# Kernel optimization log

Hardware: AMD Instinct MI355X
Metric: run time of the kernel (lower is better)

Reference implementation:

```python
import jax, jax.numpy as jnp
import numpy as np

B = 128
NHEAD = 16
D_MODEL = 512
D_IN = 256  # each of f_* and f_*_out; concat -> 512
N_ATOM = 128


def _scopes():
    lens = np.array([96 + (i % 33) for i in range(B)], dtype=np.int64)  # max == 128 == N_ATOM
    starts_a = np.concatenate([[1], 1 + np.cumsum(lens)[:-1]]).astype(np.int64)
    nb = 2 * lens
    starts_b = np.concatenate([[1], 1 + np.cumsum(nb)[:-1]]).astype(np.int64)
    return lens, starts_a, nb, starts_b


def setup_inputs() -> dict:
    key = jax.random.key(0)
    ks = jax.random.split(key, 10)
    lens, starts_a, nb, starts_b = _scopes()
    Na = int(1 + lens.sum())   # 14279 (row 0 is padding)
    Nb = int(1 + nb.sum())     # 28557 (bond 0 is padding)
    f_atoms = jax.random.normal(ks[0], (Na, D_IN), jnp.float32)
    f_bonds = jax.random.normal(ks[1], (Nb, D_IN), jnp.float32)
    f_atoms_out = jax.random.normal(ks[2], (Na, D_IN), jnp.float32)
    f_bonds_out = jax.random.normal(ks[3], (Nb, D_IN), jnp.float32)
    b2a = jax.random.randint(ks[4], (Nb,), 0, 96, jnp.int64 if jax.config.jax_enable_x64 else jnp.int32)
    b2revb = jax.random.randint(ks[5], (Nb,), 0, Nb, b2a.dtype)
    a_scope = jnp.stack([jnp.asarray(starts_a), jnp.asarray(lens)], axis=1)
    b_scope = jnp.stack([jnp.asarray(starts_b), jnp.asarray(nb)], axis=1)
    W_atom = jax.random.normal(ks[6], (2 * D_IN, D_MODEL), jnp.float32) * 0.02
    b_atom = jnp.zeros((D_MODEL,), jnp.float32)
    W_bond = jax.random.normal(ks[7], (2 * D_IN, NHEAD), jnp.float32) * 0.02
    b_bond = jnp.zeros((NHEAD,), jnp.float32)
    return {"f_atoms": f_atoms, "f_bonds": f_bonds, "f_atoms_out": f_atoms_out,
            "f_bonds_out": f_bonds_out, "b2a": b2a, "b2revb": b2revb,
            "a_scope": a_scope, "b_scope": b_scope, "n_atom": N_ATOM,
            "W_atom": W_atom, "b_atom": b_atom, "W_bond": W_bond, "b_bond": b_bond}


def reference(f_atoms, f_bonds, f_atoms_out, f_bonds_out, b2a, b2revb,
              a_scope, b_scope, n_atom, W_atom, b_atom, W_bond, b_bond):
    Bsz = a_scope.shape[0]
    # atom embedding: concat + linear, drop padding row 0, pad per-molecule -> [n_atom, B, d]
    atoms = jnp.concatenate([f_atoms, f_atoms_out], axis=1) @ W_atom + b_atom  # [Na, d]
    starts_a, lens_a = a_scope[:, 0], a_scope[:, 1]
    pos = jnp.arange(n_atom)
    valid = pos[None, :] < lens_a[:, None]                       # [B, n_atom]
    gidx = jnp.where(valid, starts_a[:, None] + pos[None, :], 0)  # safe gather idx
    atoms_pad = jnp.where(valid[..., None], atoms[gidx], 0.0)     # [B, n_atom, d]
    atoms_emb = atoms_pad.transpose(1, 0, 2)                      # [n_atom, B, d] (batch_first=False)
    # bond embedding -> scatter into dense pairwise matrix
    bonds = jnp.concatenate([f_bonds, f_bonds_out], axis=1) @ W_bond + b_bond  # [Nb, nhead]
    Nb = bonds.shape[0]
    starts_b = b_scope[:, 0]
    mol = jnp.searchsorted(starts_b, jnp.arange(Nb), side='right') - 1  # molecule id per bond (-1 for pad bond 0)
    offset = jnp.maximum(mol, 0) * (n_atom * n_atom)
    idx = b2a + b2a[b2revb] * n_atom + offset                     # flat index into [B*n_atom*n_atom]
    flat = jnp.zeros((Bsz * n_atom * n_atom, bonds.shape[1]), bonds.dtype).at[idx].set(bonds)
    apairs = flat.reshape(Bsz, n_atom, n_atom, -1)                # [B, n_atom, n_atom, nhead]
    padding_mask = ~valid                                         # [B, n_atom], True = pad
    apairs = jnp.where(padding_mask[:, None, :, None], -jnp.inf, apairs)
    apairs = apairs.transpose(0, 3, 1, 2)                         # [B, nhead, n_atom, n_atom]
    return atoms_emb, apairs, padding_mask
```

## Files before the change

### kernel.cpp

```cpp
#include <hip/hip_runtime.h>
#include <math.h>

#define NEG_BIG (-1e30f)

typedef __attribute__((ext_vector_type(8))) short short8;
typedef __attribute__((ext_vector_type(8))) _Float16 half8;
typedef __attribute__((ext_vector_type(4))) float floatx4;

__device__ __forceinline__ unsigned short f2bf(float x) {
    unsigned u = __float_as_uint(x);
    unsigned r = (u + 0x7fffu + ((u >> 16) & 1u)) >> 16;
    return (unsigned short)r;
}
__device__ __forceinline__ short f2h(float x) {
    _Float16 h = (_Float16)x;
    return __builtin_bit_cast(short, h);
}
__device__ __forceinline__ float h2f(short s) {
    return (float)__builtin_bit_cast(_Float16, s);
}

__global__ __launch_bounds__(256) void k_prep(
    const float* __restrict__ W, short* __restrict__ H, short* __restrict__ L,
    const float* __restrict__ Wb, short* __restrict__ Wbt,
    int* __restrict__ winner,
    const int* __restrict__ a_scope, float* __restrict__ mask_out, int Bmol)
{
    int bid = blockIdx.x;
    int tid = threadIdx.x;
    if (bid < 1024) {
        int t = bid * 256 + tid;
        int n = t >> 9, k = t & 511;
        float x = W[(size_t)k * 512 + n];
        short h = f2h(x);
        float r = (x - h2f(h)) * 2048.0f;
        H[t] = h;
        L[t] = f2h(r);
        return;
    }
    bid -= 1024;
    if (bid < 32) {
        int t = bid * 256 + tid;
        int h = t >> 9, k = t & 511;
        Wbt[t] = (short)f2bf(Wb[(size_t)k * 16 + h]);
        return;
    }
    bid -= 32;
    if (bid < Bmol * 16) {
        int t = bid * 256 + tid;
        ((int4*)winner)[t] = make_int4(-1, -1, -1, -1);
        return;
    }
    bid -= Bmol * 16;
    {
        int t = bid * 256 + tid;
        if (t < Bmol * 128) {
            int b = t >> 7, p = t & 127;
            mask_out[t] = (p >= a_scope[2 * b + 1]) ? 1.0f : 0.0f;
        }
    }
}


__device__ __forceinline__ void atoms_body(
    int abid, char* smem,
    const float* __restrict__ fA, const float* __restrict__ fAo,
    const int* __restrict__ a_scope,
    const short* __restrict__ WH, const short* __restrict__ WL,
    const float* __restrict__ bias, float* __restrict__ out, int Bmol)
{
    short* A_s = (short*)smem;
    short* B_s = (short*)(smem + 20480);
    int*   rs  = (int*)(smem + 40960);

    const int tid = threadIdx.x;
    const int n0 = (abid & 3) * 128;
    const int mol = abid >> 2;

    if (tid < 128) {
        int len = a_scope[2 * mol + 1];
        rs[tid] = (tid < len) ? (a_scope[2 * mol] + tid) : -1;
    }
    const int wid = tid >> 6, lane = tid & 63;
    const int wm = (wid >> 1) * 64, wn = (wid & 1) * 64;
    const int quad = lane >> 4, l16 = lane & 15;

    floatx4 acc1[4][4], acc2[4][4];
#pragma unroll
    for (int i = 0; i < 4; i++)
#pragma unroll
        for (int j = 0; j < 4; j++) {
            acc1[i][j] = (floatx4){0.f, 0.f, 0.f, 0.f};
            acc2[i][j] = (floatx4){0.f, 0.f, 0.f, 0.f};
        }

    const int ar = tid >> 1;
    const int ak = (tid & 1) * 16;
    __syncthreads();
    const int asrc = rs[ar];

    for (int k0 = 0; k0 < 512; k0 += 32) {
        float x[16];
        if (asrc >= 0) {
            int kg = k0 + ak;
            const float* p = (kg < 256) ? (fA + (size_t)asrc * 256 + kg)
                                        : (fAo + (size_t)asrc * 256 + (kg - 256));
#pragma unroll
            for (int i = 0; i < 4; i++) {
                float4 v = ((const float4*)p)[i];
                x[i * 4 + 0] = v.x; x[i * 4 + 1] = v.y;
                x[i * 4 + 2] = v.z; x[i * 4 + 3] = v.w;
            }
        } else {
#pragma unroll
            for (int i = 0; i < 16; i++) x[i] = 0.f;
        }
        size_t goff = (size_t)(n0 + ar) * 512 + k0 + ak;
        short8 bh0 = *(const short8*)(WH + goff);
        short8 bh1 = *(const short8*)(WH + goff + 8);
        short8 bl0 = *(const short8*)(WL + goff);
        short8 bl1 = *(const short8*)(WL + goff + 8);

        short8 ah0, ah1, al0, al1;
#pragma unroll
        for (int i = 0; i < 8; i++) {
            short h = f2h(x[i]);
            float r = (x[i] - h2f(h)) * 2048.0f;
            ah0[i] = h; al0[i] = f2h(r);
        }
#pragma unroll
        for (int i = 0; i < 8; i++) {
            float xx = x[8 + i];
            short h = f2h(xx);
            float r = (xx - h2f(h)) * 2048.0f;
            ah1[i] = h; al1[i] = f2h(r);
        }

        __syncthreads();
        const int abase = ar * 40 + ak;
        *(short8*)&A_s[abase] = ah0;          *(short8*)&A_s[abase + 8] = ah1;
        *(short8*)&A_s[5120 + abase] = al0;   *(short8*)&A_s[5120 + abase + 8] = al1;
        *(short8*)&B_s[abase] = bh0;          *(short8*)&B_s[abase + 8] = bh1;
        *(short8*)&B_s[5120 + abase] = bl0;   *(short8*)&B_s[5120 + abase + 8] = bl1;
        __syncthreads();

        half8 afh[4], afl[4];
#pragma unroll
        for (int ti = 0; ti < 4; ti++) {
            int off = (wm + ti * 16 + l16) * 40 + quad * 8;
            afh[ti] = *(const half8*)&A_s[off];
            afl[ti] = *(const half8*)&A_s[5120 + off];
        }
#pragma unroll
        for (int tj = 0; tj < 4; tj++) {
            int off = (wn + tj * 16 + l16) * 40 + quad * 8;
            half8 bh = *(const half8*)&B_s[off];
            half8 bl = *(const half8*)&B_s[5120 + off];
#pragma unroll
            for (int ti = 0; ti < 4; ti++) {
                acc1[ti][tj] = __builtin_amdgcn_mfma_f32_16x16x32_f16(afh[ti], bh, acc1[ti][tj], 0, 0, 0);
                acc2[ti][tj] = __builtin_amdgcn_mfma_f32_16x16x32_f16(afh[ti], bl, acc2[ti][tj], 0, 0, 0);
                acc2[ti][tj] = __builtin_amdgcn_mfma_f32_16x16x32_f16(afl[ti], bh, acc2[ti][tj], 0, 0, 0);
            }
        }
    }

#pragma unroll
    for (int tj = 0; tj < 4; tj++) {
        int n = n0 + wn + tj * 16 + l16;
        float bv = bias[n];
#pragma unroll
        for (int ti = 0; ti < 4; ti++) {
#pragma unroll
            for (int r = 0; r < 4; r++) {
                int pos = wm + ti * 16 + quad * 4 + r;
                bool valid = rs[pos] >= 0;
                float v = valid ? (acc1[ti][tj][r] + 4.8828125e-4f * acc2[ti][tj][r] + bv) : 0.f;
                out[((size_t)pos * Bmol + mol) * 512 + n] = v;
            }
        }
    }
}

__device__ __forceinline__ void bonds_body(
    int bbid, char* smem,
    const float* __restrict__ fB, const float* __restrict__ fBo,
    const short* __restrict__ Wbt, const float* __restrict__ bb_,
    float* __restrict__ bonds, int Nb)
{
    short* feat = (short*)smem;
    short* wb   = (short*)(smem + 17408);

    const int tid = threadIdx.x;
    const int j0 = bbid * 64;

    for (int c = tid; c < 1024; c += 256) {
        int h = c >> 6, cc = c & 63;
        short8 v = *(const short8*)(Wbt + h * 512 + cc * 8);
        *(short8*)&wb[h * 512 + (((cc + h) & 63) * 8)] = v;
    }

    const int wid = tid >> 6, lane = tid & 63;
    const int quad = lane >> 4, l16 = lane & 15;
    floatx4 acc = (floatx4){0.f, 0.f, 0.f, 0.f};

    const int fr = tid >> 2;
    const int fs = (tid & 3) * 32;
    const int j = j0 + fr;

    for (int k0 = 0; k0 < 512; k0 += 128) {
        float x[32];
        if (j < Nb) {
            const float* p = (k0 < 256) ? (fB + (size_t)j * 256 + k0 + fs)
                                        : (fBo + (size_t)j * 256 + (k0 - 256) + fs);
#pragma unroll
            for (int i = 0; i < 8; i++) {
                float4 v = ((const float4*)p)[i];
                x[i * 4 + 0] = v.x; x[i * 4 + 1] = v.y;
                x[i * 4 + 2] = v.z; x[i * 4 + 3] = v.w;
            }
        } else {
#pragma unroll
            for (int i = 0; i < 32; i++) x[i] = 0.f;
        }
        __syncthreads();
#pragma unroll
        for (int c = 0; c < 4; c++) {
            short8 s;
#pragma unroll
            for (int i = 0; i < 8; i++) s[i] = (short)f2bf(x[c * 8 + i]);
            *(short8*)&feat[fr * 136 + fs + c * 8] = s;
        }
        __syncthreads();
#pragma unroll
        for (int kk = 0; kk < 4; kk++) {
            short8 a = *(const short8*)&feat[(wid * 16 + l16) * 136 + kk * 32 + quad * 8];
            int kchunk = (k0 + kk * 32 + quad * 8) >> 3;
            short8 b = *(const short8*)&wb[l16 * 512 + (((kchunk + l16) & 63) * 8)];
            acc = __builtin_amdgcn_mfma_f32_16x16x32_bf16(a, b, acc, 0, 0, 0);
        }
    }
    float bv = bb_[l16];
#pragma unroll
    for (int r = 0; r < 4; r++) {
        int jj = j0 + wid * 16 + quad * 4 + r;
        if (jj < Nb) bonds[(size_t)jj * 16 + l16] = acc[r] + bv;
    }
}

__device__ __forceinline__ void fill_body(
    int fbid, const int* __restrict__ a_scope, float* __restrict__ out_ap)
{
    int f = fbid * 256 + threadIdx.x;
    int r = f >> 3;
    int b = r >> 11;
    int p2b = (f & 7) * 16;
    int len = a_scope[2 * b + 1];
    float4* dst = (float4*)(out_ap + (size_t)f * 16);
#pragma unroll
    for (int c = 0; c < 4; c++) {
        float4 v;
        v.x = (p2b + c * 4 + 0 >= len) ? NEG_BIG : 0.f;
        v.y = (p2b + c * 4 + 1 >= len) ? NEG_BIG : 0.f;
        v.z = (p2b + c * 4 + 2 >= len) ? NEG_BIG : 0.f;
        v.w = (p2b + c * 4 + 3 >= len) ? NEG_BIG : 0.f;
        dst[c] = v;
    }
}

__device__ __forceinline__ void scatter_body(
    int sbid, char* smem,
    const int* __restrict__ b2a, const int* __restrict__ b2revb,
    const int* __restrict__ b_scope, int* __restrict__ winner,
    int Nb, int Bmol)
{
    int* sb = (int*)smem;
    int tid = threadIdx.x;
    if (tid < Bmol) sb[tid] = b_scope[2 * tid];
    __syncthreads();
    int j = sbid * 256 + tid;
    if (j >= Nb) return;
    int lo = 0, hi = Bmol;
    while (lo < hi) { int mid = (lo + hi) >> 1; if (sb[mid] <= j) lo = mid + 1; else hi = mid; }
    int mol = lo - 1; if (mol < 0) mol = 0;
    int p2 = b2a[j];
    int p1 = b2a[b2revb[j]];
    atomicMax(&winner[mol * 16384 + p1 * 128 + p2], j);
}

__global__ __launch_bounds__(256, 2) void k_main(
    const float* __restrict__ fA, const float* __restrict__ fAo,
    const float* __restrict__ fB, const float* __restrict__ fBo,
    const int* __restrict__ b2a, const int* __restrict__ b2revb,
    const int* __restrict__ a_scope, const int* __restrict__ b_scope,
    const short* __restrict__ WH, const short* __restrict__ WL,
    const short* __restrict__ Wbt,
    const float* __restrict__ b_atom, const float* __restrict__ b_bond,
    float* __restrict__ out_emb, float* __restrict__ out_ap,
    float* __restrict__ bonds_ws, int* __restrict__ winner,
    int Bmol, int Nb, int nAtomsB, int nBondsB, int nFillB)
{
    __shared__ char smem[41472];
    int bid = blockIdx.x;
    if (bid < nAtomsB) {
        atoms_body(bid, smem, fA, fAo, a_scope, WH, WL, b_atom, out_emb, Bmol);
        return;
    }
    bid -= nAtomsB;
    if (bid < nBondsB) {
        bonds_body(bid, smem, fB, fBo, Wbt, b_bond, bonds_ws, Nb);
        return;
    }
    bid -= nBondsB;
    if (bid < nFillB) {
        fill_body(bid, a_scope, out_ap);
        return;
    }
    bid -= nFillB;
    scatter_body(bid, smem, b2a, b2revb, b_scope, winner, Nb, Bmol);
}

__global__ __launch_bounds__(256) void k_commit(
    const int* __restrict__ b2a, const int* __restrict__ b2revb,
    const int* __restrict__ b_scope, const int* __restrict__ a_scope,
    const int* __restrict__ winner, const float* __restrict__ bonds,
    float* __restrict__ out_ap, int Nb, int Bmol)
{
    __shared__ int sb[128];
    int tid = threadIdx.x;
    if (tid < Bmol) sb[tid] = b_scope[2 * tid];
    __syncthreads();
    int j = blockIdx.x * 256 + tid;
    if (j >= Nb) return;
    int lo = 0, hi = Bmol;
    while (lo < hi) { int mid = (lo + hi) >> 1; if (sb[mid] <= j) lo = mid + 1; else hi = mid; }
    int mol = lo - 1; if (mol < 0) mol = 0;
    int p2 = b2a[j];
    int p1 = b2a[b2revb[j]];
    int cell = mol * 16384 + p1 * 128 + p2;
    if (winner[cell] != j) return;
    if (p2 >= a_scope[2 * mol + 1]) return;
    const float4* src = (const float4*)(bonds + (size_t)j * 16);
    float4 v0 = src[0], v1 = src[1], v2 = src[2], v3 = src[3];
    float vals[16] = {v0.x, v0.y, v0.z, v0.w, v1.x, v1.y, v1.z, v1.w,
                      v2.x, v2.y, v2.z, v2.w, v3.x, v3.y, v3.z, v3.w};
    float* dst = out_ap + ((size_t)mol * 16 * 128 + p1) * 128 + p2;
#pragma unroll
    for (int h = 0; h < 16; h++) dst[(size_t)h * 16384] = vals[h];
}

extern "C" void kernel_launch(void* const* d_in, const int* in_sizes, int n_in,
                              void* d_out, int out_size, void* d_ws, size_t ws_size,
                              hipStream_t stream)
{
    const float* f_atoms     = (const float*)d_in[0];
    const float* f_bonds     = (const float*)d_in[1];
    const float* f_atoms_out = (const float*)d_in[2];
    const float* f_bonds_out = (const float*)d_in[3];
    const int*   b2a         = (const int*)d_in[4];
    const int*   b2revb      = (const int*)d_in[5];
    const int*   a_scope     = (const int*)d_in[6];
    const int*   b_scope     = (const int*)d_in[7];
    const float* W_atom      = (const float*)d_in[9];
    const float* b_atom      = (const float*)d_in[10];
    const float* W_bond      = (const float*)d_in[11];
    const float* b_bond      = (const float*)d_in[12];

    const int Bmol = in_sizes[6] / 2;
    const int Nb   = in_sizes[4];

    char* ws = (char*)d_ws;
    size_t off = 0;
    float* bonds_ws = (float*)(ws + off); off += ((size_t)Nb * 16 * 4 + 255) & ~(size_t)255;
    int*   winner   = (int*)(ws + off);   off += (size_t)Bmol * 16384 * 4;
    short* WH       = (short*)(ws + off); off += 512 * 512 * 2;
    short* WL       = (short*)(ws + off); off += 512 * 512 * 2;
    short* Wbt      = (short*)(ws + off); off += 16 * 512 * 2;

    float* out_emb  = (float*)d_out;
    float* out_ap   = out_emb + (size_t)128 * Bmol * 512;
    float* out_mask = out_ap + (size_t)Bmol * 16 * 128 * 128;

    const int prepB = 1024 + 32 + Bmol * 16 + (Bmol * 128 + 255) / 256;
    hipLaunchKernelGGL(k_prep, dim3(prepB), dim3(256), 0, stream,
                       W_atom, WH, WL, W_bond, Wbt, winner, a_scope, out_mask, Bmol);

    const int nAtomsB = 4 * Bmol;
    const int nBondsB = (Nb + 63) / 64;
    const int nFillB  = Bmol * 64;
    const int nScatB  = (Nb + 255) / 256;
    hipLaunchKernelGGL(k_main, dim3(nAtomsB + nBondsB + nFillB + nScatB), dim3(256), 0, stream,
                       f_atoms, f_atoms_out, f_bonds, f_bonds_out,
                       b2a, b2revb, a_scope, b_scope,
                       WH, WL, Wbt, b_atom, b_bond,
                       out_emb, out_ap, bonds_ws, winner,
                       Bmol, Nb, nAtomsB, nBondsB, nFillB);

    hipLaunchKernelGGL(k_commit, dim3(nScatB), dim3(256), 0, stream,
                       b2a, b2revb, b_scope, a_scope, winner, bonds_ws, out_ap, Nb, Bmol);
}
```

Baseline: 332.6 us.

## Restructure into phase kernels: bonds/W-split/scatter first, atoms GEMM with fill second

Reorganizes the launch schedule. The bond GEMM, W_atom hi/lo split, scatter-winner pass and mask write now run together in a first kernel, and the atom GEMM plus -inf fill run in a second kernel. The bond GEMM converts W_bond to bf16 per block instead of using a precomputed transpose, and winner initialization moves to a memset. The commit kernel now assigns one thread per (bond, head) instead of one thread per bond. This adds a memset launch and redundant W_bond conversion per bond block in exchange for removing the prep dependency and balancing the phases.

```diff
diff --git a/kernel.cpp b/kernel.cpp
--- a/kernel.cpp
+++ b/kernel.cpp
@@ -20,172 +20,11 @@
     return (float)__builtin_bit_cast(_Float16, s);
 }
 
-__global__ __launch_bounds__(256) void k_prep(
-    const float* __restrict__ W, short* __restrict__ H, short* __restrict__ L,
-    const float* __restrict__ Wb, short* __restrict__ Wbt,
-    int* __restrict__ winner,
-    const int* __restrict__ a_scope, float* __restrict__ mask_out, int Bmol)
-{
-    int bid = blockIdx.x;
-    int tid = threadIdx.x;
-    if (bid < 1024) {
-        int t = bid * 256 + tid;
-        int n = t >> 9, k = t & 511;
-        float x = W[(size_t)k * 512 + n];
-        short h = f2h(x);
-        float r = (x - h2f(h)) * 2048.0f;
-        H[t] = h;
-        L[t] = f2h(r);
-        return;
-    }
-    bid -= 1024;
-    if (bid < 32) {
-        int t = bid * 256 + tid;
-        int h = t >> 9, k = t & 511;
-        Wbt[t] = (short)f2bf(Wb[(size_t)k * 16 + h]);
-        return;
-    }
-    bid -= 32;
-    if (bid < Bmol * 16) {
-        int t = bid * 256 + tid;
-        ((int4*)winner)[t] = make_int4(-1, -1, -1, -1);
-        return;
-    }
-    bid -= Bmol * 16;
-    {
-        int t = bid * 256 + tid;
-        if (t < Bmol * 128) {
-            int b = t >> 7, p = t & 127;
-            mask_out[t] = (p >= a_scope[2 * b + 1]) ? 1.0f : 0.0f;
-        }
-    }
-}
-
-
-__device__ __forceinline__ void atoms_body(
-    int abid, char* smem,
-    const float* __restrict__ fA, const float* __restrict__ fAo,
-    const int* __restrict__ a_scope,
-    const short* __restrict__ WH, const short* __restrict__ WL,
-    const float* __restrict__ bias, float* __restrict__ out, int Bmol)
-{
-    short* A_s = (short*)smem;
-    short* B_s = (short*)(smem + 20480);
-    int*   rs  = (int*)(smem + 40960);
-
-    const int tid = threadIdx.x;
-    const int n0 = (abid & 3) * 128;
-    const int mol = abid >> 2;
-
-    if (tid < 128) {
-        int len = a_scope[2 * mol + 1];
-        rs[tid] = (tid < len) ? (a_scope[2 * mol] + tid) : -1;
-    }
-    const int wid = tid >> 6, lane = tid & 63;
-    const int wm = (wid >> 1) * 64, wn = (wid & 1) * 64;
-    const int quad = lane >> 4, l16 = lane & 15;
-
-    floatx4 acc1[4][4], acc2[4][4];
-#pragma unroll
-    for (int i = 0; i < 4; i++)
-#pragma unroll
-        for (int j = 0; j < 4; j++) {
-            acc1[i][j] = (floatx4){0.f, 0.f, 0.f, 0.f};
-            acc2[i][j] = (floatx4){0.f, 0.f, 0.f, 0.f};
-        }
-
-    const int ar = tid >> 1;
-    const int ak = (tid & 1) * 16;
-    __syncthreads();
-    const int asrc = rs[ar];
-
-    for (int k0 = 0; k0 < 512; k0 += 32) {
-        float x[16];
-        if (asrc >= 0) {
-            int kg = k0 + ak;
-            const float* p = (kg < 256) ? (fA + (size_t)asrc * 256 + kg)
-                                        : (fAo + (size_t)asrc * 256 + (kg - 256));
-#pragma unroll
-            for (int i = 0; i < 4; i++) {
-                float4 v = ((const float4*)p)[i];
-                x[i * 4 + 0] = v.x; x[i * 4 + 1] = v.y;
-                x[i * 4 + 2] = v.z; x[i * 4 + 3] = v.w;
-            }
-        } else {
-#pragma unroll
-            for (int i = 0; i < 16; i++) x[i] = 0.f;
-        }
-        size_t goff = (size_t)(n0 + ar) * 512 + k0 + ak;
-        short8 bh0 = *(const short8*)(WH + goff);
-        short8 bh1 = *(const short8*)(WH + goff + 8);
-        short8 bl0 = *(const short8*)(WL + goff);
-        short8 bl1 = *(const short8*)(WL + goff + 8);
-
-        short8 ah0, ah1, al0, al1;
-#pragma unroll
-        for (int i = 0; i < 8; i++) {
-            short h = f2h(x[i]);
-            float r = (x[i] - h2f(h)) * 2048.0f;
-            ah0[i] = h; al0[i] = f2h(r);
-        }
-#pragma unroll
-        for (int i = 0; i < 8; i++) {
-            float xx = x[8 + i];
-            short h = f2h(xx);
-            float r = (xx - h2f(h)) * 2048.0f;
-            ah1[i] = h; al1[i] = f2h(r);
-        }
-
-        __syncthreads();
-        const int abase = ar * 40 + ak;
-        *(short8*)&A_s[abase] = ah0;          *(short8*)&A_s[abase + 8] = ah1;
-        *(short8*)&A_s[5120 + abase] = al0;   *(short8*)&A_s[5120 + abase + 8] = al1;
-        *(short8*)&B_s[abase] = bh0;          *(short8*)&B_s[abase + 8] = bh1;
-        *(short8*)&B_s[5120 + abase] = bl0;   *(short8*)&B_s[5120 + abase + 8] = bl1;
-        __syncthreads();
-
-        half8 afh[4], afl[4];
-#pragma unroll
-        for (int ti = 0; ti < 4; ti++) {
-            int off = (wm + ti * 16 + l16) * 40 + quad * 8;
-            afh[ti] = *(const half8*)&A_s[off];
-            afl[ti] = *(const half8*)&A_s[5120 + off];
-        }
-#pragma unroll
-        for (int tj = 0; tj < 4; tj++) {
-            int off = (wn + tj * 16 + l16) * 40 + quad * 8;
-            half8 bh = *(const half8*)&B_s[off];
-            half8 bl = *(const half8*)&B_s[5120 + off];
-#pragma unroll
-            for (int ti = 0; ti < 4; ti++) {
-                acc1[ti][tj] = __builtin_amdgcn_mfma_f32_16x16x32_f16(afh[ti], bh, acc1[ti][tj], 0, 0, 0);
-                acc2[ti][tj] = __builtin_amdgcn_mfma_f32_16x16x32_f16(afh[ti], bl, acc2[ti][tj], 0, 0, 0);
-                acc2[ti][tj] = __builtin_amdgcn_mfma_f32_16x16x32_f16(afl[ti], bh, acc2[ti][tj], 0, 0, 0);
-            }
-        }
-    }
-
-#pragma unroll
-    for (int tj = 0; tj < 4; tj++) {
-        int n = n0 + wn + tj * 16 + l16;
-        float bv = bias[n];
-#pragma unroll
-        for (int ti = 0; ti < 4; ti++) {
-#pragma unroll
-            for (int r = 0; r < 4; r++) {
-                int pos = wm + ti * 16 + quad * 4 + r;
-                bool valid = rs[pos] >= 0;
-                float v = valid ? (acc1[ti][tj][r] + 4.8828125e-4f * acc2[ti][tj][r] + bv) : 0.f;
-                out[((size_t)pos * Bmol + mol) * 512 + n] = v;
-            }
-        }
-    }
-}
 
 __device__ __forceinline__ void bonds_body(
     int bbid, char* smem,
     const float* __restrict__ fB, const float* __restrict__ fBo,
-    const short* __restrict__ Wbt, const float* __restrict__ bb_,
+    const float* __restrict__ Wb_raw, const float* __restrict__ bb_,
     float* __restrict__ bonds, int Nb)
 {
     short* feat = (short*)smem;
@@ -194,10 +33,9 @@
     const int tid = threadIdx.x;
     const int j0 = bbid * 64;
 
-    for (int c = tid; c < 1024; c += 256) {
-        int h = c >> 6, cc = c & 63;
-        short8 v = *(const short8*)(Wbt + h * 512 + cc * 8);
-        *(short8*)&wb[h * 512 + (((cc + h) & 63) * 8)] = v;
+    for (int c = tid; c < 8192; c += 256) {
+        int k = c >> 4, h = c & 15;
+        wb[h * 512 + ((((k >> 3) + h) & 63) << 3) + (k & 7)] = (short)f2bf(Wb_raw[c]);
     }
 
     const int wid = tid >> 6, lane = tid & 63;
@@ -245,26 +83,6 @@
     for (int r = 0; r < 4; r++) {
         int jj = j0 + wid * 16 + quad * 4 + r;
         if (jj < Nb) bonds[(size_t)jj * 16 + l16] = acc[r] + bv;
-    }
-}
-
-__device__ __forceinline__ void fill_body(
-    int fbid, const int* __restrict__ a_scope, float* __restrict__ out_ap)
-{
-    int f = fbid * 256 + threadIdx.x;
-    int r = f >> 3;
-    int b = r >> 11;
-    int p2b = (f & 7) * 16;
-    int len = a_scope[2 * b + 1];
-    float4* dst = (float4*)(out_ap + (size_t)f * 16);
-#pragma unroll
-    for (int c = 0; c < 4; c++) {
-        float4 v;
-        v.x = (p2b + c * 4 + 0 >= len) ? NEG_BIG : 0.f;
-        v.y = (p2b + c * 4 + 1 >= len) ? NEG_BIG : 0.f;
-        v.z = (p2b + c * 4 + 2 >= len) ? NEG_BIG : 0.f;
-        v.w = (p2b + c * 4 + 3 >= len) ? NEG_BIG : 0.f;
-        dst[c] = v;
     }
 }
 
@@ -288,17 +106,196 @@
     atomicMax(&winner[mol * 16384 + p1 * 128 + p2], j);
 }
 
-__global__ __launch_bounds__(256, 2) void k_main(
+__device__ __forceinline__ void atoms_body(
+    int abid, char* smem,
     const float* __restrict__ fA, const float* __restrict__ fAo,
+    const int* __restrict__ a_scope,
+    const short* __restrict__ WH, const short* __restrict__ WL,
+    const float* __restrict__ bias, float* __restrict__ out, int Bmol)
+{
+    short* A_s = (short*)smem;
+    short* B_s = (short*)(smem + 20480);
+    int*   rs  = (int*)(smem + 40960);
+
+    const int tid = threadIdx.x;
+    const int n0 = (abid & 3) * 128;
+    const int mol = abid >> 2;
+
+    if (tid < 128) {
+        int len = a_scope[2 * mol + 1];
+        rs[tid] = (tid < len) ? (a_scope[2 * mol] + tid) : -1;
+    }
+    const int wid = tid >> 6, lane = tid & 63;
+    const int wm = (wid >> 1) * 64, wn = (wid & 1) * 64;
+    const int quad = lane >> 4, l16 = lane & 15;
+
+    floatx4 acc1[4][4], acc2[4][4];
+#pragma unroll
+    for (int i = 0; i < 4; i++)
+#pragma unroll
+        for (int j = 0; j < 4; j++) {
+            acc1[i][j] = (floatx4){0.f, 0.f, 0.f, 0.f};
+            acc2[i][j] = (floatx4){0.f, 0.f, 0.f, 0.f};
+        }
+
+    const int ar = tid >> 1;
+    const int ak = (tid & 1) * 16;
+    __syncthreads();
+    const int asrc = rs[ar];
+
+    for (int k0 = 0; k0 < 512; k0 += 32) {
+        float x[16];
+        if (asrc >= 0) {
+            int kg = k0 + ak;
+            const float* p = (kg < 256) ? (fA + (size_t)asrc * 256 + kg)
+                                        : (fAo + (size_t)asrc * 256 + (kg - 256));
+#pragma unroll
+            for (int i = 0; i < 4; i++) {
+                float4 v = ((const float4*)p)[i];
+                x[i * 4 + 0] = v.x; x[i * 4 + 1] = v.y;
+                x[i * 4 + 2] = v.z; x[i * 4 + 3] = v.w;
+            }
+        } else {
+#pragma unroll
+            for (int i = 0; i < 16; i++) x[i] = 0.f;
+        }
+        size_t goff = (size_t)(n0 + ar) * 512 + k0 + ak;
+        short8 bh0 = *(const short8*)(WH + goff);
+        short8 bh1 = *(const short8*)(WH + goff + 8);
+        short8 bl0 = *(const short8*)(WL + goff);
+        short8 bl1 = *(const short8*)(WL + goff + 8);
+
+        short8 ah0, ah1, al0, al1;
+#pragma unroll
+        for (int i = 0; i < 8; i++) {
+            short h = f2h(x[i]);
+            float r = (x[i] - h2f(h)) * 2048.0f;
+            ah0[i] = h; al0[i] = f2h(r);
+        }
+#pragma unroll
+        for (int i = 0; i < 8; i++) {
+            float xx = x[8 + i];
+            short h = f2h(xx);
+            float r = (xx - h2f(h)) * 2048.0f;
+            ah1[i] = h; al1[i] = f2h(r);
+        }
+
+        __syncthreads();
+        const int abase = ar * 40 + ak;
+        *(short8*)&A_s[abase] = ah0;          *(short8*)&A_s[abase + 8] = ah1;
+        *(short8*)&A_s[5120 + abase] = al0;   *(short8*)&A_s[5120 + abase + 8] = al1;
+        *(short8*)&B_s[abase] = bh0;          *(short8*)&B_s[abase + 8] = bh1;
+        *(short8*)&B_s[5120 + abase] = bl0;   *(short8*)&B_s[5120 + abase + 8] = bl1;
+        __syncthreads();
+
+        half8 afh[4], afl[4];
+#pragma unroll
+        for (int ti = 0; ti < 4; ti++) {
+            int off = (wm + ti * 16 + l16) * 40 + quad * 8;
+            afh[ti] = *(const half8*)&A_s[off];
+            afl[ti] = *(const half8*)&A_s[5120 + off];
+        }
+#pragma unroll
+        for (int tj = 0; tj < 4; tj++) {
+            int off = (wn + tj * 16 + l16) * 40 + quad * 8;
+            half8 bh = *(const half8*)&B_s[off];
+            half8 bl = *(const half8*)&B_s[5120 + off];
+#pragma unroll
+            for (int ti = 0; ti < 4; ti++) {
+                acc1[ti][tj] = __builtin_amdgcn_mfma_f32_16x16x32_f16(afh[ti], bh, acc1[ti][tj], 0, 0, 0);
+                acc2[ti][tj] = __builtin_amdgcn_mfma_f32_16x16x32_f16(afh[ti], bl, acc2[ti][tj], 0, 0, 0);
+                acc2[ti][tj] = __builtin_amdgcn_mfma_f32_16x16x32_f16(afl[ti], bh, acc2[ti][tj], 0, 0, 0);
+            }
+        }
+    }
+
+#pragma unroll
+    for (int tj = 0; tj < 4; tj++) {
+        int n = n0 + wn + tj * 16 + l16;
+        float bv = bias[n];
+#pragma unroll
+        for (int ti = 0; ti < 4; ti++) {
+#pragma unroll
+            for (int r = 0; r < 4; r++) {
+                int pos = wm + ti * 16 + quad * 4 + r;
+                bool valid = rs[pos] >= 0;
+                float v = valid ? (acc1[ti][tj][r] + 4.8828125e-4f * acc2[ti][tj][r] + bv) : 0.f;
+                out[((size_t)pos * Bmol + mol) * 512 + n] = v;
+            }
+        }
+    }
+}
+
+__device__ __forceinline__ void fill_body(
+    int fbid, const int* __restrict__ a_scope, float* __restrict__ out_ap)
+{
+    int f = fbid * 256 + threadIdx.x;
+    int r = f >> 3;
+    int b = r >> 11;
+    int p2b = (f & 7) * 16;
+    int len = a_scope[2 * b + 1];
+    float4* dst = (float4*)(out_ap + (size_t)f * 16);
+#pragma unroll
+    for (int c = 0; c < 4; c++) {
+        float4 v;
+        v.x = (p2b + c * 4 + 0 >= len) ? NEG_BIG : 0.f;
+        v.y = (p2b + c * 4 + 1 >= len) ? NEG_BIG : 0.f;
+        v.z = (p2b + c * 4 + 2 >= len) ? NEG_BIG : 0.f;
+        v.w = (p2b + c * 4 + 3 >= len) ? NEG_BIG : 0.f;
+        dst[c] = v;
+    }
+}
+
+__global__ __launch_bounds__(256) void k_phase1(
     const float* __restrict__ fB, const float* __restrict__ fBo,
+    const float* __restrict__ Wb_raw, const float* __restrict__ b_bond,
+    float* __restrict__ bonds_ws, int Nb,
+    const float* __restrict__ W, short* __restrict__ WH, short* __restrict__ WL,
     const int* __restrict__ b2a, const int* __restrict__ b2revb,
-    const int* __restrict__ a_scope, const int* __restrict__ b_scope,
+    const int* __restrict__ b_scope, int* __restrict__ winner,
+    const int* __restrict__ a_scope, float* __restrict__ mask_out,
+    int Bmol, int nBondsB, int nScatB)
+{
+    __shared__ char smem[33792];
+    int bid = blockIdx.x;
+    int tid = threadIdx.x;
+    if (bid < nBondsB) {
+        bonds_body(bid, smem, fB, fBo, Wb_raw, b_bond, bonds_ws, Nb);
+        return;
+    }
+    bid -= nBondsB;
+    if (bid < 1024) {
+        int t = bid * 256 + tid;
+        int n = t >> 9, k = t & 511;
+        float x = W[(size_t)k * 512 + n];
+        short h = f2h(x);
+        float r = (x - h2f(h)) * 2048.0f;
+        WH[t] = h;
+        WL[t] = f2h(r);
+        return;
+    }
+    bid -= 1024;
+    if (bid < nScatB) {
+        scatter_body(bid, smem, b2a, b2revb, b_scope, winner, Nb, Bmol);
+        return;
+    }
+    bid -= nScatB;
+    {
+        int t = bid * 256 + tid;
+        if (t < Bmol * 128) {
+            int b = t >> 7, p = t & 127;
+            mask_out[t] = (p >= a_scope[2 * b + 1]) ? 1.0f : 0.0f;
+        }
+    }
+}
+
+__global__ __launch_bounds__(256, 2) void k_phase2(
+    const float* __restrict__ fA, const float* __restrict__ fAo,
+    const int* __restrict__ a_scope,
     const short* __restrict__ WH, const short* __restrict__ WL,
-    const short* __restrict__ Wbt,
-    const float* __restrict__ b_atom, const float* __restrict__ b_bond,
+    const float* __restrict__ b_atom,
     float* __restrict__ out_emb, float* __restrict__ out_ap,
-    float* __restrict__ bonds_ws, int* __restrict__ winner,
-    int Bmol, int Nb, int nAtomsB, int nBondsB, int nFillB)
+    int Bmol, int nAtomsB)
 {
     __shared__ char smem[41472];
     int bid = blockIdx.x;
@@ -306,18 +303,7 @@
         atoms_body(bid, smem, fA, fAo, a_scope, WH, WL, b_atom, out_emb, Bmol);
         return;
     }
-    bid -= nAtomsB;
-    if (bid < nBondsB) {
-        bonds_body(bid, smem, fB, fBo, Wbt, b_bond, bonds_ws, Nb);
-        return;
-    }
-    bid -= nBondsB;
-    if (bid < nFillB) {
-        fill_body(bid, a_scope, out_ap);
-        return;
-    }
-    bid -= nFillB;
-    scatter_body(bid, smem, b2a, b2revb, b_scope, winner, Nb, Bmol);
+    fill_body(bid - nAtomsB, a_scope, out_ap);
 }
 
 __global__ __launch_bounds__(256) void k_commit(
@@ -330,7 +316,8 @@
     int tid = threadIdx.x;
     if (tid < Bmol) sb[tid] = b_scope[2 * tid];
     __syncthreads();
-    int j = blockIdx.x * 256 + tid;
+    int t = blockIdx.x * 256 + tid;
+    int j = t >> 4, h = t & 15;
     if (j >= Nb) return;
     int lo = 0, hi = Bmol;
     while (lo < hi) { int mid = (lo + hi) >> 1; if (sb[mid] <= j) lo = mid + 1; else hi = mid; }
@@ -340,13 +327,7 @@
     int cell = mol * 16384 + p1 * 128 + p2;
     if (winner[cell] != j) return;
     if (p2 >= a_scope[2 * mol + 1]) return;
-    const float4* src = (const float4*)(bonds + (size_t)j * 16);
-    float4 v0 = src[0], v1 = src[1], v2 = src[2], v3 = src[3];
-    float vals[16] = {v0.x, v0.y, v0.z, v0.w, v1.x, v1.y, v1.z, v1.w,
-                      v2.x, v2.y, v2.z, v2.w, v3.x, v3.y, v3.z, v3.w};
-    float* dst = out_ap + ((size_t)mol * 16 * 128 + p1) * 128 + p2;
-#pragma unroll
-    for (int h = 0; h < 16; h++) dst[(size_t)h * 16384] = vals[h];
+    out_ap[(((size_t)mol * 16 + h) * 128 + p1) * 128 + p2] = bonds[(size_t)j * 16 + h];
 }
 
 extern "C" void kernel_launch(void* const* d_in, const int* in_sizes, int n_in,
@@ -375,27 +356,28 @@
     int*   winner   = (int*)(ws + off);   off += (size_t)Bmol * 16384 * 4;
     short* WH       = (short*)(ws + off); off += 512 * 512 * 2;
     short* WL       = (short*)(ws + off); off += 512 * 512 * 2;
-    short* Wbt      = (short*)(ws + off); off += 16 * 512 * 2;
 
     float* out_emb  = (float*)d_out;
     float* out_ap   = out_emb + (size_t)128 * Bmol * 512;
     float* out_mask = out_ap + (size_t)Bmol * 16 * 128 * 128;
 
-    const int prepB = 1024 + 32 + Bmol * 16 + (Bmol * 128 + 255) / 256;
-    hipLaunchKernelGGL(k_prep, dim3(prepB), dim3(256), 0, stream,
-                       W_atom, WH, WL, W_bond, Wbt, winner, a_scope, out_mask, Bmol);
+    hipMemsetAsync(winner, 0xFF, (size_t)Bmol * 16384 * 4, stream);
+
+    const int nBondsB = (Nb + 63) / 64;
+    const int nScatB  = (Nb + 255) / 256;
+    const int nMaskB  = (Bmol * 128 + 255) / 256;
+    hipLaunchKernelGGL(k_phase1, dim3(nBondsB + 1024 + nScatB + nMaskB), dim3(256), 0, stream,
+                       f_bonds, f_bonds_out, W_bond, b_bond, bonds_ws, Nb,
+                       W_atom, WH, WL,
+                       b2a, b2revb, b_scope, winner,
+                       a_scope, out_mask, Bmol, nBondsB, nScatB);
 
     const int nAtomsB = 4 * Bmol;
-    const int nBondsB = (Nb + 63) / 64;
     const int nFillB  = Bmol * 64;
-    const int nScatB  = (Nb + 255) / 256;
-    hipLaunchKernelGGL(k_main, dim3(nAtomsB + nBondsB + nFillB + nScatB), dim3(256), 0, stream,
-                       f_atoms, f_atoms_out, f_bonds, f_bonds_out,
-                       b2a, b2revb, a_scope, b_scope,
-                       WH, WL, Wbt, b_atom, b_bond,
-                       out_emb, out_ap, bonds_ws, winner,
-                       Bmol, Nb, nAtomsB, nBondsB, nFillB);
-
-    hipLaunchKernelGGL(k_commit, dim3(nScatB), dim3(256), 0, stream,
+    hipLaunchKernelGGL(k_phase2, dim3(nAtomsB + nFillB), dim3(256), 0, stream,
+                       f_atoms, f_atoms_out, a_scope, WH, WL, b_atom,
+                       out_emb, out_ap, Bmol, nAtomsB);
+
+    hipLaunchKernelGGL(k_commit, dim3((Nb * 16 + 255) / 256), dim3(256), 0, stream,
                        b2a, b2revb, b_scope, a_scope, winner, bonds_ws, out_ap, Nb, Bmol);
 }
```

Measured after the change: 334.0 us. No clear change (+0.4%).
